# Kernel optimization log

Measured on AMD Instinct MI355X. Metric: run time of the kernel, lower is better.

Reference implementation:

```python
import jax, jax.numpy as jnp
import numpy as np

PE_SIZE = 16          # sqrt(num_patches=256)
HIDDEN_STRIDE = 2
CUBIC_A = -0.75       # torch bicubic coefficient


def cubic_resize_matrix(in_size, out_size, a=CUBIC_A):
    """(out_size, in_size) weights for torch bicubic, align_corners=False."""
    dst = np.arange(out_size)
    src = (dst + 0.5) * in_size / out_size - 0.5
    x0 = np.floor(src).astype(np.int64)
    W = np.zeros((out_size, in_size), np.float32)
    for k in range(-1, 3):  # 4 taps
        idx = np.clip(x0 + k, 0, in_size - 1)  # border replicate
        d = np.abs(src - (x0 + k))
        w = np.where(d <= 1.0, (a + 2) * d**3 - (a + 3) * d**2 + 1.0,
            np.where(d < 2.0, a * d**3 - 5 * a * d**2 + 8 * a * d - 4 * a, 0.0))
        np.add.at(W, (dst, idx), w.astype(np.float32))
    return W


def setup_inputs() -> dict:
    key = jax.random.key(0)
    k1, k2, k3, k4 = jax.random.split(key, 4)
    n_img, t, h, w = 8, 1, 64, 64
    total = n_img * t * h * w  # 32768 patches
    in_feat, d = 3 * 14 * 14, 1152
    return {
        "pixel_values": jax.random.normal(k1, (total, in_feat), jnp.float32),
        "w_patch": jax.random.normal(k2, (d, in_feat), jnp.float32) * 0.02,
        "b_patch": jax.random.normal(k3, (d,), jnp.float32) * 0.02,
        "pos_table": jax.random.normal(k4, (PE_SIZE * PE_SIZE, d), jnp.float32) * 0.02,
        "grid_thws": jnp.array([[t, h, w]] * n_img, jnp.int64),
    }


def _pos_embed(pos_table, grid):
    """grid: np int array (n_img, 3) -> (sum t*h*w, d) positional embeddings."""
    d = pos_table.shape[-1]
    pe_grid = pos_table.reshape(PE_SIZE, PE_SIZE, d)  # (H, W, d)
    s = HIDDEN_STRIDE
    pieces = []
    for t, h, w in grid:
        Wh = jnp.asarray(cubic_resize_matrix(PE_SIZE, int(h)))
        Ww = jnp.asarray(cubic_resize_matrix(PE_SIZE, int(w)))
        pe = jnp.einsum('hH,wW,HWd->hwd', Wh, Ww, pe_grid)  # (h, w, d)
        # hidden_stride window rearrange: (h,w,d) -> (h/s, w/s, s, s, d)
        pe = pe.reshape(h // s, s, w // s, s, d).transpose(0, 2, 1, 3, 4)
        pe = pe.reshape(h * w, d)
        pe = jnp.tile(pe, (int(t), 1))  # repeat over temporal dim
        pieces.append(pe)
    return jnp.concatenate(pieces, axis=0)


def reference(pixel_values, w_patch, b_patch, pos_table, grid_thws):
    # patch embedding (Linear)
    patch_embeds = pixel_values @ w_patch.T + b_patch  # (N, d)
    grid = np.asarray(grid_thws)  # static shapes per image
    pos = _pos_embed(pos_table, grid)
    return patch_embeds + pos
```

## Files before the change

kernel.cpp:

```cpp
#include <hip/hip_runtime.h>

typedef unsigned short ushort_t;
typedef unsigned int uint_t;

typedef __bf16 bf16x8 __attribute__((ext_vector_type(8)));
typedef float f32x4 __attribute__((ext_vector_type(4)));

#define KK 588
#define KP 608
#define NN 1152
#define MM 32768
#define POSROWS 4096
#define NSTEP 19
#define GRID 2304
#define CHUNKS_PER_ROW 76


__device__ __forceinline__ void cubic_taps(int dst, float* w, int* idx) {
    const float A = -0.75f;
    float src = (float)dst * 0.25f - 0.25f;
    int x0 = (int)floorf(src);
    #pragma unroll
    for (int k = -1; k <= 2; ++k) {
        int i = x0 + k;
        int ic = i < 0 ? 0 : (i > 15 ? 15 : i);
        float d = fabsf(src - (float)i);
        float wt;
        if (d <= 1.0f)      wt = ((A + 2.0f) * d - (A + 3.0f)) * d * d + 1.0f;
        else if (d < 2.0f)  wt = ((A * d - 5.0f * A) * d + 8.0f * A) * d - 4.0f * A;
        else                wt = 0.0f;
        w[k + 1] = wt;
        idx[k + 1] = ic;
    }
}


__global__ void pos_kernel(const float* __restrict__ pt, float* __restrict__ pos) {
    int n = blockIdx.x;
    int h = ((n >> 7) << 1) | ((n >> 1) & 1);
    int w = (((n >> 2) & 31) << 1) | (n & 1);
    float wh[4], ww[4];
    int ih[4], iw[4];
    cubic_taps(h, wh, ih);
    cubic_taps(w, ww, iw);
    int tid = threadIdx.x;
    if (tid >= NN / 4) return;
    const f32x4* pt4 = (const f32x4*)pt;
    f32x4 s = {0.f, 0.f, 0.f, 0.f};
    #pragma unroll
    for (int a = 0; a < 4; ++a) {
        #pragma unroll
        for (int b = 0; b < 4; ++b) {
            float wt = wh[a] * ww[b];
            f32x4 v = pt4[(ih[a] * 16 + iw[b]) * (NN / 4) + tid];
            s.x += wt * v.x; s.y += wt * v.y; s.z += wt * v.z; s.w += wt * v.w;
        }
    }
    ((f32x4*)pos)[(size_t)n * (NN / 4) + tid] = s;
}


__global__ void cvt_pad_kernel(const float* __restrict__ src, ushort_t* __restrict__ dst,
                               int rows) {
    int c = blockIdx.x * 256 + threadIdx.x;
    if (c >= rows * CHUNKS_PER_ROW) return;
    int row = c / CHUNKS_PER_ROW;
    int k0 = (c - row * CHUNKS_PER_ROW) * 8;
    const float* g = src + (size_t)row * KK + k0;
    bf16x8 v;
    if (k0 + 8 <= KK) {
        f32x4 a = *(const f32x4*)g;
        f32x4 b = *(const f32x4*)(g + 4);
        #pragma unroll
        for (int e = 0; e < 4; ++e) { v[e] = (__bf16)a[e]; v[e + 4] = (__bf16)b[e]; }
    } else {
        #pragma unroll
        for (int e = 0; e < 8; ++e)
            v[e] = (k0 + e < KK) ? (__bf16)g[e] : (__bf16)0.f;
    }
    *(bf16x8*)(dst + (size_t)row * KP + k0) = v;
}


__global__ void gemm_kernel(const ushort_t* __restrict__ Abf,
                            const ushort_t* __restrict__ Bbf,
                            const float* __restrict__ bias,
                            const float* __restrict__ pos,
                            float* __restrict__ out) {
    __shared__ __align__(16) ushort_t lA[3][128 * 32];
    __shared__ __align__(16) ushort_t lB[3][128 * 32];

    const int t = threadIdx.x;
    const int lane = t & 63;
    const int wid = t >> 6;
    const int wm = wid >> 1, wn = wid & 1;

    int linear = (int)blockIdx.x;
    int xcd = linear & 7;
    int local = linear >> 3;
    int wg = xcd * (GRID / 8) + local;
    int mt = wg / 9;
    int nt = wg - mt * 9;
    const int bm = mt * 128;
    const int bn = nt * 128;

    f32x4 acc[4][4] = {};

    auto stage = [&](int ks, int buf) {
        const int k0 = ks * 32;
        #pragma unroll
        for (int j = 0; j < 2; ++j) {
            int idx = j * 256 + t;
            int row = idx >> 2;
            int slot = idx & 3;
            int khi = slot ^ ((row >> 1) & 3);
            const ushort_t* gA = Abf + (size_t)(bm + row) * KP + k0 + khi * 8;
            const ushort_t* gB = Bbf + (size_t)(bn + row) * KP + k0 + khi * 8;
            ushort_t* lAp = &lA[buf][(size_t)(idx & ~63) * 8];
            ushort_t* lBp = &lB[buf][(size_t)(idx & ~63) * 8];
            __builtin_amdgcn_global_load_lds(
                (const __attribute__((address_space(1))) void*)gA,
                (__attribute__((address_space(3))) void*)lAp, 16, 0, 0);
            __builtin_amdgcn_global_load_lds(
                (const __attribute__((address_space(1))) void*)gB,
                (__attribute__((address_space(3))) void*)lBp, 16, 0, 0);
        }
    };

    stage(0, 0);
    stage(1, 1);

    for (int ks = 0; ks < NSTEP; ++ks) {
        const int cur = ks % 3;

        if (ks + 2 < NSTEP) {
            stage(ks + 2, (ks + 2) % 3);
            asm volatile("s_waitcnt vmcnt(8)" ::: "memory");
        } else if (ks + 1 < NSTEP) {
            asm volatile("s_waitcnt vmcnt(4)" ::: "memory");
        } else {
            asm volatile("s_waitcnt vmcnt(0)" ::: "memory");
        }
        __builtin_amdgcn_s_barrier();
        __builtin_amdgcn_sched_barrier(0);

        bf16x8 af[4], bfr[4];
        #pragma unroll
        for (int mi = 0; mi < 4; ++mi) {
            int row = wm * 64 + mi * 16 + (lane & 15);
            int slot = (lane >> 4) ^ ((row >> 1) & 3);
            af[mi] = *(const bf16x8*)(&lA[cur][row * 32 + slot * 8]);
        }
        #pragma unroll
        for (int ni = 0; ni < 4; ++ni) {
            int row = wn * 64 + ni * 16 + (lane & 15);
            int slot = (lane >> 4) ^ ((row >> 1) & 3);
            bfr[ni] = *(const bf16x8*)(&lB[cur][row * 32 + slot * 8]);
        }
        #pragma unroll
        for (int mi = 0; mi < 4; ++mi)
            #pragma unroll
            for (int ni = 0; ni < 4; ++ni)
                acc[mi][ni] = __builtin_amdgcn_mfma_f32_16x16x32_bf16(
                    af[mi], bfr[ni], acc[mi][ni], 0, 0, 0);

        asm volatile("s_waitcnt lgkmcnt(0)" ::: "memory");
        __builtin_amdgcn_s_barrier();
    }

    #pragma unroll
    for (int mi = 0; mi < 4; ++mi) {
        #pragma unroll
        for (int ni = 0; ni < 4; ++ni) {
            int col = bn + wn * 64 + ni * 16 + (lane & 15);
            float bcol = bias[col];
            #pragma unroll
            for (int r = 0; r < 4; ++r) {
                int row = bm + wm * 64 + mi * 16 + (lane >> 4) * 4 + r;
                int prow = row & (POSROWS - 1);
                out[(size_t)row * NN + col] =
                    acc[mi][ni][r] + bcol + pos[(size_t)prow * NN + col];
            }
        }
    }
}


__global__ void fb_kernel(const float* __restrict__ A, const float* __restrict__ W,
                          const float* __restrict__ bias, const float* __restrict__ pt,
                          float* __restrict__ out) {
    __shared__ float sA[16][17], sB[16][17];
    int ty = threadIdx.y, tx = threadIdx.x;
    int row = blockIdx.y * 16 + ty;
    int col = blockIdx.x * 16 + tx;
    float acc = 0.f;
    for (int k0 = 0; k0 < KK; k0 += 16) {
        int ka = k0 + tx;
        sA[ty][tx] = (ka < KK) ? A[(size_t)row * KK + ka] : 0.f;
        sB[ty][tx] = (ka < KK) ? W[(size_t)(blockIdx.x * 16 + ty) * KK + ka] : 0.f;
        __syncthreads();
        #pragma unroll
        for (int kk = 0; kk < 16; ++kk)
            acc += sA[ty][kk] * sB[tx][kk];
        __syncthreads();
    }
    int n = row & (POSROWS - 1);
    int h = ((n >> 7) << 1) | ((n >> 1) & 1);
    int w = (((n >> 2) & 31) << 1) | (n & 1);
    float wh[4], ww[4]; int ih[4], iw[4];
    cubic_taps(h, wh, ih);
    cubic_taps(w, ww, iw);
    float p = 0.f;
    #pragma unroll
    for (int a = 0; a < 4; ++a) {
        float rs = 0.f;
        #pragma unroll
        for (int b = 0; b < 4; ++b)
            rs += ww[b] * pt[(ih[a] * 16 + iw[b]) * NN + col];
        p += wh[a] * rs;
    }
    out[(size_t)row * NN + col] = acc + bias[col] + p;
}


extern "C" void kernel_launch(void* const* d_in, const int* in_sizes, int n_in,
                              void* d_out, int out_size, void* d_ws, size_t ws_size,
                              hipStream_t stream) {
    const float* pv   = (const float*)d_in[0];
    const float* wp   = (const float*)d_in[1];
    const float* bias = (const float*)d_in[2];
    const float* pt   = (const float*)d_in[3];
    float* out = (float*)d_out;

    const size_t pos_bytes = (size_t)POSROWS * NN * 4;
    const size_t pvb_bytes = (size_t)MM * KP * 2;
    const size_t wb_bytes  = (size_t)NN * KP * 2;
    const size_t need = pos_bytes + pvb_bytes + wb_bytes;

    if (ws_size >= need) {
        float* pos = (float*)d_ws;
        ushort_t* pvb = (ushort_t*)((char*)d_ws + pos_bytes);
        ushort_t* wb  = (ushort_t*)((char*)d_ws + pos_bytes + pvb_bytes);

        pos_kernel<<<POSROWS, 320, 0, stream>>>(pt, pos);

        int ca = MM * CHUNKS_PER_ROW;
        cvt_pad_kernel<<<(ca + 255) / 256, 256, 0, stream>>>(pv, pvb, MM);
        int cb = NN * CHUNKS_PER_ROW;
        cvt_pad_kernel<<<(cb + 255) / 256, 256, 0, stream>>>(wp, wb, NN);

        gemm_kernel<<<GRID, 256, 0, stream>>>(pvb, wb, bias, pos, out);
    } else {
        fb_kernel<<<dim3(NN / 16, MM / 16), dim3(16, 16), 0, stream>>>(pv, wp, bias, pt, out);
    }
}
```

Measured before the change: 131.9 us.

## Enlarge GEMM tile to 256x128, swap MFMA operands for vector epilogue, fuse cvt launches

Doubles the M tile of the bf16 GEMM to 256 rows, so each wave computes 128x64 and the grid halves. This raises operand reuse and cuts B-tile reloads. The MFMA operands are swapped so each lane holds 4 consecutive columns, which lets the bias+pos epilogue use float4 loads and stores. LDS reads are split into groups with staged lgkmcnt waits and setprio so MFMAs can overlap the reads, and the two convert kernels are merged into one launch. The cost is more registers and LDS per block, which may lower occupancy, and fewer blocks to spread across the CUs.

```diff
diff --git a/kernel.cpp b/kernel.cpp
--- a/kernel.cpp
+++ b/kernel.cpp
@@ -12,7 +12,9 @@
 #define MM 32768
 #define POSROWS 4096
 #define NSTEP 19
-#define GRID 2304
+#define BM 256
+#define BN 128
+#define GRID 1152
 #define CHUNKS_PER_ROW 76
 
 
@@ -60,10 +62,18 @@
 }
 
 
-__global__ void cvt_pad_kernel(const float* __restrict__ src, ushort_t* __restrict__ dst,
-                               int rows) {
+__global__ void cvt_pad_kernel(const float* __restrict__ srcA, ushort_t* __restrict__ dstA,
+                               const float* __restrict__ srcB, ushort_t* __restrict__ dstB) {
     int c = blockIdx.x * 256 + threadIdx.x;
-    if (c >= rows * CHUNKS_PER_ROW) return;
+    const int ca = MM * CHUNKS_PER_ROW;
+    const float* src;
+    ushort_t* dst;
+    if (c < ca) { src = srcA; dst = dstA; }
+    else {
+        c -= ca;
+        if (c >= NN * CHUNKS_PER_ROW) return;
+        src = srcB; dst = dstB;
+    }
     int row = c / CHUNKS_PER_ROW;
     int k0 = (c - row * CHUNKS_PER_ROW) * 8;
     const float* g = src + (size_t)row * KK + k0;
@@ -82,16 +92,19 @@
 }
 
 
-__global__ void gemm_kernel(const ushort_t* __restrict__ Abf,
-                            const ushort_t* __restrict__ Bbf,
-                            const float* __restrict__ bias,
-                            const float* __restrict__ pos,
-                            float* __restrict__ out) {
-    __shared__ __align__(16) ushort_t lA[3][128 * 32];
-    __shared__ __align__(16) ushort_t lB[3][128 * 32];
+__global__ __launch_bounds__(256, 2)
+void gemm_kernel(const ushort_t* __restrict__ Abf,
+                 const ushort_t* __restrict__ Bbf,
+                 const float* __restrict__ bias,
+                 const float* __restrict__ pos,
+                 float* __restrict__ out) {
+    __shared__ __align__(16) ushort_t lA[3][BM * 32];
+    __shared__ __align__(16) ushort_t lB[3][BN * 32];
 
     const int t = threadIdx.x;
     const int lane = t & 63;
+    const int lm = lane & 15;
+    const int lq = (lane >> 4);
     const int wid = t >> 6;
     const int wm = wid >> 1, wn = wid & 1;
 
@@ -101,26 +114,33 @@
     int wg = xcd * (GRID / 8) + local;
     int mt = wg / 9;
     int nt = wg - mt * 9;
-    const int bm = mt * 128;
-    const int bn = nt * 128;
-
-    f32x4 acc[4][4] = {};
+    const int bm = mt * BM;
+    const int bn = nt * BN;
+
+    f32x4 acc[8][4] = {};
 
     auto stage = [&](int ks, int buf) {
         const int k0 = ks * 32;
+        #pragma unroll
+        for (int j = 0; j < 4; ++j) {
+            int idx = j * 256 + t;
+            int row = idx >> 2;
+            int slot = idx & 3;
+            int khi = slot ^ ((row >> 1) & 3);
+            const ushort_t* gA = Abf + (size_t)(bm + row) * KP + k0 + khi * 8;
+            ushort_t* lAp = &lA[buf][(size_t)(idx & ~63) * 8];
+            __builtin_amdgcn_global_load_lds(
+                (const __attribute__((address_space(1))) void*)gA,
+                (__attribute__((address_space(3))) void*)lAp, 16, 0, 0);
+        }
         #pragma unroll
         for (int j = 0; j < 2; ++j) {
             int idx = j * 256 + t;
             int row = idx >> 2;
             int slot = idx & 3;
             int khi = slot ^ ((row >> 1) & 3);
-            const ushort_t* gA = Abf + (size_t)(bm + row) * KP + k0 + khi * 8;
             const ushort_t* gB = Bbf + (size_t)(bn + row) * KP + k0 + khi * 8;
-            ushort_t* lAp = &lA[buf][(size_t)(idx & ~63) * 8];
             ushort_t* lBp = &lB[buf][(size_t)(idx & ~63) * 8];
-            __builtin_amdgcn_global_load_lds(
-                (const __attribute__((address_space(1))) void*)gA,
-                (__attribute__((address_space(3))) void*)lAp, 16, 0, 0);
             __builtin_amdgcn_global_load_lds(
                 (const __attribute__((address_space(1))) void*)gB,
                 (__attribute__((address_space(3))) void*)lBp, 16, 0, 0);
@@ -135,52 +155,81 @@
 
         if (ks + 2 < NSTEP) {
             stage(ks + 2, (ks + 2) % 3);
-            asm volatile("s_waitcnt vmcnt(8)" ::: "memory");
+            asm volatile("s_waitcnt vmcnt(12)" ::: "memory");
         } else if (ks + 1 < NSTEP) {
-            asm volatile("s_waitcnt vmcnt(4)" ::: "memory");
+            asm volatile("s_waitcnt vmcnt(6)" ::: "memory");
         } else {
             asm volatile("s_waitcnt vmcnt(0)" ::: "memory");
         }
         __builtin_amdgcn_s_barrier();
         __builtin_amdgcn_sched_barrier(0);
 
-        bf16x8 af[4], bfr[4];
-        #pragma unroll
-        for (int mi = 0; mi < 4; ++mi) {
-            int row = wm * 64 + mi * 16 + (lane & 15);
-            int slot = (lane >> 4) ^ ((row >> 1) & 3);
+        bf16x8 af[8], bfr[4];
+        #pragma unroll
+        for (int ni = 0; ni < 4; ++ni) {
+            int row = wn * 64 + ni * 16 + lm;
+            int slot = lq ^ ((row >> 1) & 3);
+            bfr[ni] = *(const bf16x8*)(&lB[cur][row * 32 + slot * 8]);
+        }
+        #pragma unroll
+        for (int mi = 0; mi < 2; ++mi) {
+            int row = wm * 128 + mi * 16 + lm;
+            int slot = lq ^ ((row >> 1) & 3);
             af[mi] = *(const bf16x8*)(&lA[cur][row * 32 + slot * 8]);
         }
+        __builtin_amdgcn_sched_barrier(0);
+        #pragma unroll
+        for (int g = 1; g < 4; ++g) {
+            #pragma unroll
+            for (int mi = 2 * g; mi < 2 * g + 2; ++mi) {
+                int row = wm * 128 + mi * 16 + lm;
+                int slot = lq ^ ((row >> 1) & 3);
+                af[mi] = *(const bf16x8*)(&lA[cur][row * 32 + slot * 8]);
+            }
+            __builtin_amdgcn_sched_barrier(0);
+        }
+
+        #pragma unroll
+        for (int c = 0; c < 4; ++c) {
+            if (c == 0)      asm volatile("s_waitcnt lgkmcnt(6)" ::: "memory");
+            else if (c == 1) asm volatile("s_waitcnt lgkmcnt(4)" ::: "memory");
+            else if (c == 2) asm volatile("s_waitcnt lgkmcnt(2)" ::: "memory");
+            else             asm volatile("s_waitcnt lgkmcnt(0)" ::: "memory");
+            __builtin_amdgcn_sched_barrier(0);
+            __builtin_amdgcn_s_setprio(1);
+            #pragma unroll
+            for (int mi = 2 * c; mi < 2 * c + 2; ++mi)
+                #pragma unroll
+                for (int ni = 0; ni < 4; ++ni)
+                    acc[mi][ni] = __builtin_amdgcn_mfma_f32_16x16x32_bf16(
+                        bfr[ni], af[mi], acc[mi][ni], 0, 0, 0);
+            __builtin_amdgcn_s_setprio(0);
+        }
+        __builtin_amdgcn_sched_barrier(0);
+        __builtin_amdgcn_s_barrier();
+    }
+
+    const int N0 = bn + wn * 64;
+    const int M0 = bm + wm * 128;
+    f32x4 bias4[4];
+    #pragma unroll
+    for (int ni = 0; ni < 4; ++ni)
+        bias4[ni] = *(const f32x4*)(bias + N0 + ni * 16 + lq * 4);
+    #pragma unroll
+    for (int mi = 0; mi < 8; ++mi) {
+        int m = M0 + mi * 16 + lm;
+        const float* posrow = pos + (size_t)(m & (POSROWS - 1)) * NN;
+        float* outrow = out + (size_t)m * NN;
         #pragma unroll
         for (int ni = 0; ni < 4; ++ni) {
-            int row = wn * 64 + ni * 16 + (lane & 15);
-            int slot = (lane >> 4) ^ ((row >> 1) & 3);
-            bfr[ni] = *(const bf16x8*)(&lB[cur][row * 32 + slot * 8]);
-        }
-        #pragma unroll
-        for (int mi = 0; mi < 4; ++mi)
-            #pragma unroll
-            for (int ni = 0; ni < 4; ++ni)
-                acc[mi][ni] = __builtin_amdgcn_mfma_f32_16x16x32_bf16(
-                    af[mi], bfr[ni], acc[mi][ni], 0, 0, 0);
-
-        asm volatile("s_waitcnt lgkmcnt(0)" ::: "memory");
-        __builtin_amdgcn_s_barrier();
-    }
-
-    #pragma unroll
-    for (int mi = 0; mi < 4; ++mi) {
-        #pragma unroll
-        for (int ni = 0; ni < 4; ++ni) {
-            int col = bn + wn * 64 + ni * 16 + (lane & 15);
-            float bcol = bias[col];
-            #pragma unroll
-            for (int r = 0; r < 4; ++r) {
-                int row = bm + wm * 64 + mi * 16 + (lane >> 4) * 4 + r;
-                int prow = row & (POSROWS - 1);
-                out[(size_t)row * NN + col] =
-                    acc[mi][ni][r] + bcol + pos[(size_t)prow * NN + col];
-            }
+            int nb = N0 + ni * 16 + lq * 4;
+            f32x4 p = *(const f32x4*)(posrow + nb);
+            f32x4 v = acc[mi][ni];
+            v.x += bias4[ni].x + p.x;
+            v.y += bias4[ni].y + p.y;
+            v.z += bias4[ni].z + p.z;
+            v.w += bias4[ni].w + p.w;
+            *(f32x4*)(outrow + nb) = v;
         }
     }
 }
@@ -244,10 +293,8 @@
 
         pos_kernel<<<POSROWS, 320, 0, stream>>>(pt, pos);
 
-        int ca = MM * CHUNKS_PER_ROW;
-        cvt_pad_kernel<<<(ca + 255) / 256, 256, 0, stream>>>(pv, pvb, MM);
-        int cb = NN * CHUNKS_PER_ROW;
-        cvt_pad_kernel<<<(cb + 255) / 256, 256, 0, stream>>>(wp, wb, NN);
+        int chunks = (MM + NN) * CHUNKS_PER_ROW;
+        cvt_pad_kernel<<<(chunks + 255) / 256, 256, 0, stream>>>(pv, pvb, wp, wb);
 
         gemm_kernel<<<GRID, 256, 0, stream>>>(pvb, wb, bias, pos, out);
     } else {
```

After: 145.4 us. +10.2%, slower.

## Fuse activation fp32-to-bf16 conversion into GEMM A-tile loads and merge prep kernels

Applied to the files above, without the earlier changes.

The GEMM now reads fp32 pixel_values directly, converting to bf16 in registers and writing the A tile into LDS (double-buffered, register-prefetched two steps ahead), instead of running a separate conversion pass over the whole activation matrix. Weight conversion and positional-embedding precompute (now with bias folded in) are merged into one prep kernel. The epilogue swaps MFMA operand order so each lane stores contiguous float4 rows. This removes a large activation write and re-read and two launches, but doubles global A-load bytes inside the GEMM and adds VGPR pressure and conversion work on the critical loop.

```diff
diff --git a/kernel.cpp b/kernel.cpp
--- a/kernel.cpp
+++ b/kernel.cpp
@@ -14,6 +14,8 @@
 #define NSTEP 19
 #define GRID 2304
 #define CHUNKS_PER_ROW 76
+#define BCHUNKS (NN * CHUNKS_PER_ROW)
+#define BBLOCKS ((BCHUNKS + 255) / 256)
 
 
 __device__ __forceinline__ void cubic_taps(int dst, float* w, int* idx) {
@@ -35,65 +37,74 @@
 }
 
 
-__global__ void pos_kernel(const float* __restrict__ pt, float* __restrict__ pos) {
-    int n = blockIdx.x;
-    int h = ((n >> 7) << 1) | ((n >> 1) & 1);
-    int w = (((n >> 2) & 31) << 1) | (n & 1);
-    float wh[4], ww[4];
-    int ih[4], iw[4];
-    cubic_taps(h, wh, ih);
-    cubic_taps(w, ww, iw);
-    int tid = threadIdx.x;
-    if (tid >= NN / 4) return;
-    const f32x4* pt4 = (const f32x4*)pt;
-    f32x4 s = {0.f, 0.f, 0.f, 0.f};
-    #pragma unroll
-    for (int a = 0; a < 4; ++a) {
-        #pragma unroll
-        for (int b = 0; b < 4; ++b) {
-            float wt = wh[a] * ww[b];
-            f32x4 v = pt4[(ih[a] * 16 + iw[b]) * (NN / 4) + tid];
-            s.x += wt * v.x; s.y += wt * v.y; s.z += wt * v.z; s.w += wt * v.w;
-        }
-    }
-    ((f32x4*)pos)[(size_t)n * (NN / 4) + tid] = s;
-}
-
-
-__global__ void cvt_pad_kernel(const float* __restrict__ src, ushort_t* __restrict__ dst,
-                               int rows) {
-    int c = blockIdx.x * 256 + threadIdx.x;
-    if (c >= rows * CHUNKS_PER_ROW) return;
-    int row = c / CHUNKS_PER_ROW;
-    int k0 = (c - row * CHUNKS_PER_ROW) * 8;
-    const float* g = src + (size_t)row * KK + k0;
-    bf16x8 v;
-    if (k0 + 8 <= KK) {
-        f32x4 a = *(const f32x4*)g;
-        f32x4 b = *(const f32x4*)(g + 4);
-        #pragma unroll
-        for (int e = 0; e < 4; ++e) { v[e] = (__bf16)a[e]; v[e + 4] = (__bf16)b[e]; }
+__global__ void prep_kernel(const float* __restrict__ wp, ushort_t* __restrict__ wb,
+                            const float* __restrict__ pt, const float* __restrict__ bias,
+                            float* __restrict__ pos) {
+    int b = blockIdx.x;
+    if (b < BBLOCKS) {
+        int c = b * 256 + threadIdx.x;
+        if (c >= BCHUNKS) return;
+        int row = c / CHUNKS_PER_ROW;
+        int k0 = (c - row * CHUNKS_PER_ROW) * 8;
+        const float* g = wp + (size_t)row * KK + k0;
+        bf16x8 v;
+        if (k0 + 8 <= KK) {
+            f32x4 a = *(const f32x4*)g;
+            f32x4 bb = *(const f32x4*)(g + 4);
+            #pragma unroll
+            for (int e = 0; e < 4; ++e) { v[e] = (__bf16)a[e]; v[e + 4] = (__bf16)bb[e]; }
+        } else {
+            #pragma unroll
+            for (int e = 0; e < 8; ++e)
+                v[e] = (k0 + e < KK) ? (__bf16)g[e] : (__bf16)0.f;
+        }
+        *(bf16x8*)(wb + (size_t)row * KP + k0) = v;
     } else {
-        #pragma unroll
-        for (int e = 0; e < 8; ++e)
-            v[e] = (k0 + e < KK) ? (__bf16)g[e] : (__bf16)0.f;
-    }
-    *(bf16x8*)(dst + (size_t)row * KP + k0) = v;
-}
-
-
-__global__ void gemm_kernel(const ushort_t* __restrict__ Abf,
-                            const ushort_t* __restrict__ Bbf,
-                            const float* __restrict__ bias,
-                            const float* __restrict__ pos,
-                            float* __restrict__ out) {
-    __shared__ __align__(16) ushort_t lA[3][128 * 32];
+        int n = b - BBLOCKS;
+        int h = ((n >> 7) << 1) | ((n >> 1) & 1);
+        int w = (((n >> 2) & 31) << 1) | (n & 1);
+        float wh[4], ww[4];
+        int ih[4], iw[4];
+        cubic_taps(h, wh, ih);
+        cubic_taps(w, ww, iw);
+        const f32x4* pt4 = (const f32x4*)pt;
+        const f32x4* bias4 = (const f32x4*)bias;
+        for (int j = threadIdx.x; j < NN / 4; j += blockDim.x) {
+            f32x4 s = bias4[j];
+            #pragma unroll
+            for (int a = 0; a < 4; ++a) {
+                #pragma unroll
+                for (int bq = 0; bq < 4; ++bq) {
+                    float wt = wh[a] * ww[bq];
+                    f32x4 vv = pt4[(ih[a] * 16 + iw[bq]) * (NN / 4) + j];
+                    s.x += wt * vv.x; s.y += wt * vv.y; s.z += wt * vv.z; s.w += wt * vv.w;
+                }
+            }
+            ((f32x4*)pos)[(size_t)n * (NN / 4) + j] = s;
+        }
+    }
+}
+
+
+__global__ __launch_bounds__(256, 3)
+void gemm_kernel(const float* __restrict__ A,
+                 const ushort_t* __restrict__ Bbf,
+                 const float* __restrict__ pos,
+                 float* __restrict__ out) {
+    __shared__ __align__(16) ushort_t lA[2][128 * 32];
     __shared__ __align__(16) ushort_t lB[3][128 * 32];
 
     const int t = threadIdx.x;
     const int lane = t & 63;
+    const int lm = lane & 15;
+    const int lq = lane >> 4;
     const int wid = t >> 6;
     const int wm = wid >> 1, wn = wid & 1;
+
+    const int arow = t >> 1;
+    const int akh = (t & 1) * 16;
+    const int asw = (arow >> 1) & 3;
+    const int aq0 = (t & 1) * 2;
 
     int linear = (int)blockIdx.x;
     int xcd = linear & 7;
@@ -105,8 +116,35 @@
     const int bn = nt * 128;
 
     f32x4 acc[4][4] = {};
-
-    auto stage = [&](int ks, int buf) {
+    f32x4 rA0[4], rA1[4];
+
+    auto loadA_fast = [&](int ks, f32x4* r) {
+        const float* g = A + (size_t)(bm + arow) * KK + ks * 32 + akh;
+        r[0] = *(const f32x4*)g;
+        r[1] = *(const f32x4*)(g + 4);
+        r[2] = *(const f32x4*)(g + 8);
+        r[3] = *(const f32x4*)(g + 12);
+    };
+    auto loadA_guard = [&](int ks, f32x4* r) {
+        const float* gr = A + (size_t)(bm + arow) * KK;
+        int kb = ks * 32 + akh;
+        #pragma unroll
+        for (int e = 0; e < 16; ++e) {
+            int k = kb + e;
+            r[e >> 2][e & 3] = (k < KK) ? gr[k] : 0.f;
+        }
+    };
+    auto cvtwrA = [&](int tile, const f32x4* r) {
+        bf16x8 v0, v1;
+        #pragma unroll
+        for (int e = 0; e < 4; ++e) { v0[e] = (__bf16)r[0][e]; v0[e + 4] = (__bf16)r[1][e]; }
+        #pragma unroll
+        for (int e = 0; e < 4; ++e) { v1[e] = (__bf16)r[2][e]; v1[e + 4] = (__bf16)r[3][e]; }
+        ushort_t* base = &lA[tile & 1][arow * 32];
+        *(bf16x8*)(base + (aq0 ^ asw) * 8) = v0;
+        *(bf16x8*)(base + ((aq0 + 1) ^ asw) * 8) = v1;
+    };
+    auto stageB = [&](int ks, int buf) {
         const int k0 = ks * 32;
         #pragma unroll
         for (int j = 0; j < 2; ++j) {
@@ -114,73 +152,102 @@
             int row = idx >> 2;
             int slot = idx & 3;
             int khi = slot ^ ((row >> 1) & 3);
-            const ushort_t* gA = Abf + (size_t)(bm + row) * KP + k0 + khi * 8;
             const ushort_t* gB = Bbf + (size_t)(bn + row) * KP + k0 + khi * 8;
-            ushort_t* lAp = &lA[buf][(size_t)(idx & ~63) * 8];
             ushort_t* lBp = &lB[buf][(size_t)(idx & ~63) * 8];
-            __builtin_amdgcn_global_load_lds(
-                (const __attribute__((address_space(1))) void*)gA,
-                (__attribute__((address_space(3))) void*)lAp, 16, 0, 0);
             __builtin_amdgcn_global_load_lds(
                 (const __attribute__((address_space(1))) void*)gB,
                 (__attribute__((address_space(3))) void*)lBp, 16, 0, 0);
         }
     };
 
-    stage(0, 0);
-    stage(1, 1);
-
-    for (int ks = 0; ks < NSTEP; ++ks) {
-        const int cur = ks % 3;
-
-        if (ks + 2 < NSTEP) {
-            stage(ks + 2, (ks + 2) % 3);
-            asm volatile("s_waitcnt vmcnt(8)" ::: "memory");
-        } else if (ks + 1 < NSTEP) {
-            asm volatile("s_waitcnt vmcnt(4)" ::: "memory");
-        } else {
-            asm volatile("s_waitcnt vmcnt(0)" ::: "memory");
-        }
-        __builtin_amdgcn_s_barrier();
+    auto step = [&](int ks, f32x4* rload, f32x4* rcvt) {
+        const bool issue = (ks + 2 < NSTEP);
+        if (issue) {
+            if (ks + 2 == NSTEP - 1) loadA_guard(ks + 2, rload);
+            else                     loadA_fast(ks + 2, rload);
+            stageB(ks + 2, (ks + 2) % 3);
+        }
         __builtin_amdgcn_sched_barrier(0);
 
         bf16x8 af[4], bfr[4];
+        const ushort_t* bufA = lA[ks & 1];
+        const ushort_t* bufB = lB[ks % 3];
         #pragma unroll
         for (int mi = 0; mi < 4; ++mi) {
-            int row = wm * 64 + mi * 16 + (lane & 15);
-            int slot = (lane >> 4) ^ ((row >> 1) & 3);
-            af[mi] = *(const bf16x8*)(&lA[cur][row * 32 + slot * 8]);
+            int row = wm * 64 + mi * 16 + lm;
+            int slot = lq ^ ((row >> 1) & 3);
+            af[mi] = *(const bf16x8*)(bufA + row * 32 + slot * 8);
         }
         #pragma unroll
         for (int ni = 0; ni < 4; ++ni) {
-            int row = wn * 64 + ni * 16 + (lane & 15);
-            int slot = (lane >> 4) ^ ((row >> 1) & 3);
-            bfr[ni] = *(const bf16x8*)(&lB[cur][row * 32 + slot * 8]);
+            int row = wn * 64 + ni * 16 + lm;
+            int slot = lq ^ ((row >> 1) & 3);
+            bfr[ni] = *(const bf16x8*)(bufB + row * 32 + slot * 8);
         }
         #pragma unroll
         for (int mi = 0; mi < 4; ++mi)
             #pragma unroll
             for (int ni = 0; ni < 4; ++ni)
                 acc[mi][ni] = __builtin_amdgcn_mfma_f32_16x16x32_bf16(
-                    af[mi], bfr[ni], acc[mi][ni], 0, 0, 0);
-
+                    bfr[ni], af[mi], acc[mi][ni], 0, 0, 0);
+
+        if (issue) asm volatile("s_waitcnt vmcnt(6)" ::: "memory");
+        else       asm volatile("s_waitcnt vmcnt(0)" ::: "memory");
+        if (ks + 1 < NSTEP) cvtwrA(ks + 1, rcvt);
         asm volatile("s_waitcnt lgkmcnt(0)" ::: "memory");
         __builtin_amdgcn_s_barrier();
-    }
-
+    };
+
+    loadA_fast(0, rA0); stageB(0, 0);
+    loadA_fast(1, rA1); stageB(1, 1);
+    asm volatile("s_waitcnt vmcnt(6)" ::: "memory");
+    cvtwrA(0, rA0);
+    asm volatile("s_waitcnt lgkmcnt(0)" ::: "memory");
+    __builtin_amdgcn_s_barrier();
+
+    for (int ks = 0; ks < NSTEP - 2; ks += 2) {
+        step(ks, rA0, rA1);
+        step(ks + 1, rA1, rA0);
+    }
+
+    {
+        bf16x8 af[4], bfr[4];
+        const ushort_t* bufA = lA[0];
+        const ushort_t* bufB = lB[0];
+        #pragma unroll
+        for (int mi = 0; mi < 4; ++mi) {
+            int row = wm * 64 + mi * 16 + lm;
+            int slot = lq ^ ((row >> 1) & 3);
+            af[mi] = *(const bf16x8*)(bufA + row * 32 + slot * 8);
+        }
+        #pragma unroll
+        for (int ni = 0; ni < 4; ++ni) {
+            int row = wn * 64 + ni * 16 + lm;
+            int slot = lq ^ ((row >> 1) & 3);
+            bfr[ni] = *(const bf16x8*)(bufB + row * 32 + slot * 8);
+        }
+        #pragma unroll
+        for (int mi = 0; mi < 4; ++mi)
+            #pragma unroll
+            for (int ni = 0; ni < 4; ++ni)
+                acc[mi][ni] = __builtin_amdgcn_mfma_f32_16x16x32_bf16(
+                    bfr[ni], af[mi], acc[mi][ni], 0, 0, 0);
+    }
+
+    const int M0 = bm + wm * 64;
+    const int N0 = bn + wn * 64;
     #pragma unroll
     for (int mi = 0; mi < 4; ++mi) {
+        int m = M0 + mi * 16 + lm;
+        const float* posrow = pos + (size_t)(m & (POSROWS - 1)) * NN;
+        float* outrow = out + (size_t)m * NN;
         #pragma unroll
         for (int ni = 0; ni < 4; ++ni) {
-            int col = bn + wn * 64 + ni * 16 + (lane & 15);
-            float bcol = bias[col];
-            #pragma unroll
-            for (int r = 0; r < 4; ++r) {
-                int row = bm + wm * 64 + mi * 16 + (lane >> 4) * 4 + r;
-                int prow = row & (POSROWS - 1);
-                out[(size_t)row * NN + col] =
-                    acc[mi][ni][r] + bcol + pos[(size_t)prow * NN + col];
-            }
+            int nb = N0 + ni * 16 + lq * 4;
+            f32x4 p = *(const f32x4*)(posrow + nb);
+            f32x4 v = acc[mi][ni];
+            v.x += p.x; v.y += p.y; v.z += p.z; v.w += p.w;
+            *(f32x4*)(outrow + nb) = v;
         }
     }
 }
@@ -233,23 +300,15 @@
     float* out = (float*)d_out;
 
     const size_t pos_bytes = (size_t)POSROWS * NN * 4;
-    const size_t pvb_bytes = (size_t)MM * KP * 2;
     const size_t wb_bytes  = (size_t)NN * KP * 2;
-    const size_t need = pos_bytes + pvb_bytes + wb_bytes;
+    const size_t need = pos_bytes + wb_bytes;
 
     if (ws_size >= need) {
         float* pos = (float*)d_ws;
-        ushort_t* pvb = (ushort_t*)((char*)d_ws + pos_bytes);
-        ushort_t* wb  = (ushort_t*)((char*)d_ws + pos_bytes + pvb_bytes);
-
-        pos_kernel<<<POSROWS, 320, 0, stream>>>(pt, pos);
-
-        int ca = MM * CHUNKS_PER_ROW;
-        cvt_pad_kernel<<<(ca + 255) / 256, 256, 0, stream>>>(pv, pvb, MM);
-        int cb = NN * CHUNKS_PER_ROW;
-        cvt_pad_kernel<<<(cb + 255) / 256, 256, 0, stream>>>(wp, wb, NN);
-
-        gemm_kernel<<<GRID, 256, 0, stream>>>(pvb, wb, bias, pos, out);
+        ushort_t* wb = (ushort_t*)((char*)d_ws + pos_bytes);
+
+        prep_kernel<<<BBLOCKS + POSROWS, 256, 0, stream>>>(wp, wb, pt, bias, pos);
+        gemm_kernel<<<GRID, 256, 0, stream>>>(pv, wb, pos, out);
     } else {
         fb_kernel<<<dim3(NN / 16, MM / 16), dim3(16, 16), 0, stream>>>(pv, wp, bias, pt, out);
     }
```

After: 140.2 us. 6.3% more time.
